# Kernel tuning notes

Hardware: AMD Instinct MI355X
Metric: run time of the kernel (lower is better)

The kernel has to match this reference:

```python
import jax, jax.numpy as jnp
import numpy as np

B, N, K, L, H = 8, 2048, 16, 4, 8
CONV = (64, 64, 128, 256)
W_DIM, N_CODES, E_DIM, P_DIM, FF = 512, 8, 64, 256, 512


def act(x):
    return jax.nn.leaky_relu(x, 0.2)


def ln(x, g, b, eps=1e-5):
    m = jnp.mean(x, -1, keepdims=True)
    v = jnp.mean((x - m) ** 2, -1, keepdims=True)
    return g * (x - m) / jnp.sqrt(v + eps) + b


# per-batch neighbor gather: f [C,N], i [N,K] -> [C,N,K]
gather_nb = jax.vmap(lambda f, i: f[:, i])


def knn_idx(y):  # y [B,3,N] -> [B,N,K]
    xx = jnp.sum(y * y, axis=1)
    inner = jnp.einsum('bcn,bcm->bnm', y, y)
    dist = 2.0 * inner - xx[:, :, None] - xx[:, None, :]  # negative sq dist
    return jax.lax.top_k(dist, K)[1]


def mha(q, kv, Wq, bq, Wk, bk, Wv, bv, Wo, bo):
    Bq, S, D = q.shape
    Sk = kv.shape[1]
    dh = D // H
    qh = (q @ Wq.T + bq).reshape(Bq, S, H, dh)
    kh = (kv @ Wk.T + bk).reshape(Bq, Sk, H, dh)
    vh = (kv @ Wv.T + bv).reshape(Bq, Sk, H, dh)
    a = jax.nn.softmax(jnp.einsum('bqhd,bkhd->bhqk', qh, kh) * (1.0 / np.sqrt(dh)))
    o = jnp.einsum('bhqk,bkhd->bqhd', a, vh).reshape(Bq, S, D)
    return o @ Wo.T + bo


def setup_inputs() -> dict:
    key = jax.random.key(0)
    ks = iter(jax.random.split(key, 48))
    nrm = lambda shape: jax.random.normal(next(ks), shape, jnp.float32) * 0.02
    d = {
        'x': jax.random.normal(next(ks), (B, N, 3), jnp.float32),
        'W_ec': nrm((CONV[0], 6)), 'b_ec': jnp.zeros((CONV[0],), jnp.float32),
        'Wc1': nrm((CONV[1], CONV[0])), 'bc1': jnp.zeros((CONV[1],), jnp.float32),
        'Wc2': nrm((CONV[2], CONV[1])), 'bc2': jnp.zeros((CONV[2],), jnp.float32),
        'Wc3': nrm((CONV[3], CONV[2])), 'bc3': jnp.zeros((CONV[3],), jnp.float32),
        'Wf': nrm((W_DIM, sum(CONV))), 'bf': jnp.zeros((W_DIM,), jnp.float32),
        'Wpc': nrm((P_DIM, E_DIM)), 'bpc': jnp.zeros((P_DIM,), jnp.float32),
        'Wpi': nrm((P_DIM, 3)), 'bpi': jnp.zeros((P_DIM,), jnp.float32),
        'Wq': nrm((L, 2, P_DIM, P_DIM)), 'bq': jnp.zeros((L, 2, P_DIM), jnp.float32),
        'Wk': nrm((L, 2, P_DIM, P_DIM)), 'bk': jnp.zeros((L, 2, P_DIM), jnp.float32),
        'Wv': nrm((L, 2, P_DIM, P_DIM)), 'bv': jnp.zeros((L, 2, P_DIM), jnp.float32),
        'Wo': nrm((L, 2, P_DIM, P_DIM)), 'bo': jnp.zeros((L, 2, P_DIM), jnp.float32),
        'ln1g': jnp.ones((L, P_DIM), jnp.float32), 'ln1b': jnp.zeros((L, P_DIM), jnp.float32),
        'ln2g': jnp.ones((L, P_DIM), jnp.float32), 'ln2b': jnp.zeros((L, P_DIM), jnp.float32),
        'Wff1': nrm((L, FF, P_DIM)), 'bff1': jnp.zeros((L, FF), jnp.float32),
        'Wff2': nrm((L, P_DIM, FF)), 'bff2': jnp.zeros((L, P_DIM), jnp.float32),
        'ln3g': jnp.ones((L, P_DIM), jnp.float32), 'ln3b': jnp.zeros((L, P_DIM), jnp.float32),
        'lnfg': jnp.ones((P_DIM,), jnp.float32), 'lnfb': jnp.zeros((P_DIM,), jnp.float32),
        'Wcm': nrm((E_DIM, P_DIM)), 'bcm': jnp.zeros((E_DIM,), jnp.float32),
    }
    return d


def reference(x, W_ec, b_ec, Wc1, bc1, Wc2, bc2, Wc3, bc3, Wf, bf, Wpc, bpc, Wpi, bpi,
              Wq, bq, Wk, bk, Wv, bv, Wo, bo, ln1g, ln1b, ln2g, ln2b,
              Wff1, bff1, Wff2, bff2, ln3g, ln3b, lnfg, lnfb, Wcm, bcm):
    y = jnp.transpose(x, (0, 2, 1))                      # [B,3,N]
    idx = knn_idx(y)                                     # [B,N,K]
    nb = gather_nb(y, idx)                               # [B,3,N,K]
    feats = jnp.concatenate([nb - y[..., None], jnp.broadcast_to(y[..., None], nb.shape)], axis=1)
    h = act(jnp.einsum('oc,bcnk->bonk', W_ec, feats) + b_ec[:, None, None])
    h = h.max(axis=3)                                    # [B,64,N]
    xs = [h]
    for Wl, bl in ((Wc1, bc1), (Wc2, bc2), (Wc3, bc3)):
        h = gather_nb(h, idx).max(axis=3)                # graph max pooling
        h = act(jnp.einsum('oc,bcn->bon', Wl, h) + bl[:, None])
        xs.append(h)
    h = jnp.concatenate(xs, axis=1)                      # [B,512,N]
    h = jnp.einsum('oc,bcn->bon', Wf, h) + bf[:, None]
    xm = h.max(axis=2)                                   # [B,512]
    q = act(xm.reshape(B, N_CODES, E_DIM) @ Wpc.T + bpc) # [B,8,256]
    mem = act(x @ Wpi.T + bpi)                           # [B,N,256]
    for l in range(L):
        q = ln(q + mha(q, q, Wq[l, 0], bq[l, 0], Wk[l, 0], bk[l, 0], Wv[l, 0], bv[l, 0], Wo[l, 0], bo[l, 0]), ln1g[l], ln1b[l])
        q = ln(q + mha(q, mem, Wq[l, 1], bq[l, 1], Wk[l, 1], bk[l, 1], Wv[l, 1], bv[l, 1], Wo[l, 1], bo[l, 1]), ln2g[l], ln2b[l])
        q = ln(q + (act(q @ Wff1[l].T + bff1[l]) @ Wff2[l].T + bff2[l]), ln3g[l], ln3b[l])
    q = ln(q, lnfg, lnfb)
    out = q @ Wcm.T + bcm                                # [B,8,64]
    return out.reshape(B, W_DIM)
```

## Files before the change

### kernel.cpp

```cpp
#include <hip/hip_runtime.h>
#include <math.h>

#define BN 8
#define NP 2048
#define KNN 16
#define NL 4
#define NH 8

typedef __attribute__((ext_vector_type(8))) short bf16x8;
typedef __attribute__((ext_vector_type(4))) float f32x4;

__device__ __forceinline__ unsigned short f2bf(float f) {
    unsigned u = __float_as_uint(f);
    unsigned r = (u + 0x7FFFu + ((u >> 16) & 1u)) >> 16;
    return (unsigned short)r;
}
__device__ __forceinline__ float bf2f(unsigned short s) {
    return __uint_as_float(((unsigned)s) << 16);
}
__device__ __forceinline__ unsigned fmono(float f) {
    unsigned u = __float_as_uint(f);
    return (u & 0x80000000u) ? ~u : (u | 0x80000000u);
}
__device__ __forceinline__ float funmono(unsigned k) {
    return (k & 0x80000000u) ? __uint_as_float(k ^ 0x80000000u) : __uint_as_float(~k);
}

__device__ __forceinline__ float gemv_dot(const unsigned short* __restrict__ wrow, const float* sm, int K8) {
    const uint4* w8 = (const uint4*)wrow;
    const float4* r4 = (const float4*)sm;
    float a0 = 0.f, a1 = 0.f, a2 = 0.f, a3 = 0.f;
    #pragma unroll 8
    for (int c = 0; c < K8; ++c) {
        uint4 wv = w8[c];
        float4 x0 = r4[c * 2], x1 = r4[c * 2 + 1];
        a0 += x0.x * __uint_as_float(wv.x << 16) + x0.y * __uint_as_float(wv.x & 0xFFFF0000u);
        a1 += x0.z * __uint_as_float(wv.y << 16) + x0.w * __uint_as_float(wv.y & 0xFFFF0000u);
        a2 += x1.x * __uint_as_float(wv.z << 16) + x1.y * __uint_as_float(wv.z & 0xFFFF0000u);
        a3 += x1.z * __uint_as_float(wv.w << 16) + x1.w * __uint_as_float(wv.w & 0xFFFF0000u);
    }
    return (a0 + a1) + (a2 + a3);
}

__device__ __forceinline__ float gemv_i8(const char* __restrict__ wrow, const float* sm, int K16) {
    const uint4* w16 = (const uint4*)wrow;
    const float4* r4 = (const float4*)sm;
    float a0 = 0.f, a1 = 0.f, a2 = 0.f, a3 = 0.f;
    #pragma unroll 4
    for (int c = 0; c < K16; ++c) {
        uint4 wv = w16[c];
        float4 x0 = r4[c * 4], x1 = r4[c * 4 + 1], x2 = r4[c * 4 + 2], x3 = r4[c * 4 + 3];
        a0 += x0.x * (float)(signed char)(wv.x) + x0.y * (float)(signed char)(wv.x >> 8)
            + x0.z * (float)(signed char)(wv.x >> 16) + x0.w * (float)(signed char)(wv.x >> 24);
        a1 += x1.x * (float)(signed char)(wv.y) + x1.y * (float)(signed char)(wv.y >> 8)
            + x1.z * (float)(signed char)(wv.y >> 16) + x1.w * (float)(signed char)(wv.y >> 24);
        a2 += x2.x * (float)(signed char)(wv.z) + x2.y * (float)(signed char)(wv.z >> 8)
            + x2.z * (float)(signed char)(wv.z >> 16) + x2.w * (float)(signed char)(wv.z >> 24);
        a3 += x3.x * (float)(signed char)(wv.w) + x3.y * (float)(signed char)(wv.w >> 8)
            + x3.z * (float)(signed char)(wv.w >> 16) + x3.w * (float)(signed char)(wv.w >> 24);
    }
    return (a0 + a1) + (a2 + a3);
}

__device__ __forceinline__ unsigned long long shflx_u64(unsigned long long v, int j) {
    int lo = __shfl_xor((int)(unsigned)(v & 0xFFFFFFFFull), j);
    int hi = __shfl_xor((int)(unsigned)(v >> 32), j);
    return ((unsigned long long)(unsigned)hi << 32) | (unsigned)lo;
}

__device__ __forceinline__ unsigned sort64_u32(unsigned v, int lane) {
    #pragma unroll
    for (int k = 2; k <= 64; k <<= 1) {
        #pragma unroll
        for (int j = k >> 1; j > 0; j >>= 1) {
            unsigned o = (unsigned)__shfl_xor((int)v, j);
            bool up = ((lane & k) == 0);
            bool lower = ((lane & j) == 0);
            unsigned mn = v < o ? v : o;
            unsigned mx = v < o ? o : v;
            v = (up == lower) ? mn : mx;
        }
    }
    return v;
}

__device__ __forceinline__ unsigned long long sort64_u64(unsigned long long v, int lane) {
    #pragma unroll
    for (int k = 2; k <= 64; k <<= 1) {
        #pragma unroll
        for (int j = k >> 1; j > 0; j >>= 1) {
            unsigned long long o = shflx_u64(v, j);
            bool up = ((lane & k) == 0);
            bool lower = ((lane & j) == 0);
            unsigned long long mn = v < o ? v : o;
            unsigned long long mx = v < o ? o : v;
            v = (up == lower) ? mn : mx;
        }
    }
    return v;
}

__global__ __launch_bounds__(256) void knn_kernel(const float* __restrict__ x, int* __restrict__ idxout) {
    __shared__ float xs[2048], ys[2048], zs[2048], ns[2048];
    __shared__ unsigned long long cand[4][64];
    int tid = threadIdx.x;
    int wv = tid >> 6, lane = tid & 63;
    int p = blockIdx.x * 4 + wv;
    int b = p >> 11, n = p & 2047;
    const float* xb = x + (size_t)b * NP * 3;
    for (int t = tid; t < 2048; t += 256) {
        float mx = xb[t * 3 + 0], my = xb[t * 3 + 1], mz = xb[t * 3 + 2];
        xs[t] = mx; ys[t] = my; zs[t] = mz;
        ns[t] = mx * mx + my * my + mz * mz;
    }
    __syncthreads();
    float cx = xs[n], cy = ys[n], cz = zs[n], xn = ns[n];
    unsigned key[32];
    unsigned lmax = 0u;
    #pragma unroll
    for (int t = 0; t < 32; ++t) {
        int m = (t << 6) | lane;
        float dd = 2.0f * (cx * xs[m] + cy * ys[m] + cz * zs[m]) - xn - ns[m];
        unsigned u = __float_as_uint(dd);
        u = (u & 0x80000000u) ? ~u : (u | 0x80000000u);
        key[t] = u;
        lmax = lmax > u ? lmax : u;
    }
    unsigned sorted = sort64_u32(lmax, lane);
    unsigned S = (unsigned)__shfl((int)sorted, 48);
    int c = 0;
    #pragma unroll
    for (int t = 0; t < 32; ++t) c += (key[t] >= S) ? 1 : 0;
    int inc = c;
    #pragma unroll
    for (int d = 1; d < 64; d <<= 1) {
        int tsh = __shfl_up(inc, d);
        if (lane >= d) inc += tsh;
    }
    int C = __shfl(inc, 63);
    int* op = idxout + (size_t)p * KNN;
    if (C <= 64) {
        int off = inc - c;
        #pragma unroll
        for (int t = 0; t < 32; ++t) {
            if (key[t] >= S) {
                int m = (t << 6) | lane;
                cand[wv][off++] = ((unsigned long long)key[t] << 16) | (unsigned)(2047 - m);
            }
        }
        asm volatile("s_waitcnt lgkmcnt(0)" ::: "memory");
        unsigned long long ck = (lane < C) ? cand[wv][lane] : 0ull;
        ck = sort64_u64(ck, lane);
        if (lane >= 48) op[63 - lane] = 2047 - (int)(unsigned)(ck & 0xFFFFull);
    } else {
        unsigned taken = 0u;
        for (int r = 0; r < KNN; ++r) {
            unsigned long long best = 0ull;
            #pragma unroll
            for (int t = 0; t < 32; ++t) {
                if (!((taken >> t) & 1u)) {
                    int m = (t << 6) | lane;
                    unsigned long long ck = ((unsigned long long)key[t] << 16) | (unsigned)(2047 - m);
                    if (ck > best) best = ck;
                }
            }
            #pragma unroll
            for (int d = 1; d < 64; d <<= 1) {
                unsigned long long o = shflx_u64(best, d);
                if (o > best) best = o;
            }
            int m = 2047 - (int)(unsigned)(best & 0xFFFFull);
            if (lane == 0) op[r] = m;
            if ((m & 63) == lane) taken |= 1u << (m >> 6);
        }
    }
}

__global__ __launch_bounds__(256) void edge_conv_kernel(const float* __restrict__ x, const int* __restrict__ idx,
                                                        const float* __restrict__ Wec, const float* __restrict__ bec,
                                                        unsigned short* __restrict__ hcatT) {
    int tid = threadIdx.x;
    int g = tid >> 6, o = tid & 63;
    int p = blockIdx.x * 4 + g;
    int b = p >> 11;
    __shared__ float nb[4][KNN][3];
    __shared__ float ctr[4][3];
    if (o < KNN) {
        int j = idx[(size_t)p * KNN + o];
        const float* xp = x + ((size_t)b * NP + j) * 3;
        nb[g][o][0] = xp[0]; nb[g][o][1] = xp[1]; nb[g][o][2] = xp[2];
    }
    if (o >= KNN && o < KNN + 3) ctr[g][o - KNN] = x[(size_t)p * 3 + (o - KNN)];
    __syncthreads();
    float w0 = Wec[o * 6 + 0], w1 = Wec[o * 6 + 1], w2 = Wec[o * 6 + 2];
    float w3 = Wec[o * 6 + 3], w4 = Wec[o * 6 + 4], w5 = Wec[o * 6 + 5];
    float c0 = ctr[g][0], c1 = ctr[g][1], c2 = ctr[g][2];
    float base = bec[o] + w3 * c0 + w4 * c1 + w5 * c2;
    float m = -3.4e38f;
    #pragma unroll
    for (int k = 0; k < KNN; ++k) {
        float v = base + w0 * (nb[g][k][0] - c0) + w1 * (nb[g][k][1] - c1) + w2 * (nb[g][k][2] - c2);
        v = v > 0.f ? v : 0.2f * v;
        m = fmaxf(m, v);
    }
    hcatT[(size_t)p * 512 + o] = f2bf(m);
}

__global__ __launch_bounds__(256) void pool_bf16_kernel(const unsigned short* __restrict__ src, int s_coff,
                                                        const int* __restrict__ idx,
                                                        unsigned short* __restrict__ dst, int C) {
    int tid = threadIdx.x, wv = tid >> 6, lane = tid & 63;
    int p = blockIdx.x * 4 + wv;
    int b = p >> 11;
    const int* ip = idx + (size_t)p * KNN;
    const unsigned short* sb = src + (size_t)b * NP * 512 + s_coff;
    for (int c0 = 0; c0 < C; c0 += 64) {
        int ch = c0 + lane;
        float m = -3.4e38f;
        #pragma unroll
        for (int k = 0; k < KNN; ++k) {
            int j = ip[k];
            m = fmaxf(m, bf2f(sb[(size_t)j * 512 + ch]));
        }
        dst[(size_t)p * C + ch] = f2bf(m);
    }
}

__global__ __launch_bounds__(256) void mfma_conv64_kernel(const unsigned short* __restrict__ A,
                                                          const unsigned short* __restrict__ W,
                                                          const float* __restrict__ bias,
                                                          unsigned short* __restrict__ hcatT, int coff) {
    __shared__ unsigned short As[128][72];
    __shared__ unsigned short Bs[64][72];
    int m0 = blockIdx.x * 128, b = blockIdx.z;
    int tid = threadIdx.x;
    int lane = tid & 63, wave = tid >> 6;
    int wr = wave >> 1, wc = wave & 1;
    int quad = lane >> 4, l16 = lane & 15;
    {
        int r = tid >> 1, s = (tid & 1) * 32;
        const unsigned short* ap = A + (size_t)b * NP * 64 + (size_t)(m0 + r) * 64 + s;
        uint4 v0 = *(const uint4*)(ap);
        uint4 v1 = *(const uint4*)(ap + 8);
        uint4 v2 = *(const uint4*)(ap + 16);
        uint4 v3 = *(const uint4*)(ap + 24);
        *(uint4*)&As[r][s] = v0; *(uint4*)&As[r][s + 8] = v1;
        *(uint4*)&As[r][s + 16] = v2; *(uint4*)&As[r][s + 24] = v3;
    }
    {
        int r = tid >> 2, s = (tid & 3) * 16;
        const unsigned short* wp = W + r * 64 + s;
        *(uint4*)&Bs[r][s] = *(const uint4*)wp;
        *(uint4*)&Bs[r][s + 8] = *(const uint4*)(wp + 8);
    }
    __syncthreads();
    f32x4 acc[4][2] = {};
    #pragma unroll
    for (int k0 = 0; k0 < 64; k0 += 32) {
        bf16x8 af[4], bfv[2];
        #pragma unroll
        for (int i = 0; i < 4; ++i) af[i] = *(const bf16x8*)&As[wr * 64 + i * 16 + l16][k0 + quad * 8];
        #pragma unroll
        for (int j = 0; j < 2; ++j) bfv[j] = *(const bf16x8*)&Bs[wc * 32 + j * 16 + l16][k0 + quad * 8];
        #pragma unroll
        for (int i = 0; i < 4; ++i)
            #pragma unroll
            for (int j = 0; j < 2; ++j)
                acc[i][j] = __builtin_amdgcn_mfma_f32_16x16x32_bf16(af[i], bfv[j], acc[i][j], 0, 0, 0);
    }
    #pragma unroll
    for (int i = 0; i < 4; ++i) {
        #pragma unroll
        for (int r = 0; r < 4; ++r) {
            int pt = m0 + wr * 64 + i * 16 + quad * 4 + r;
            #pragma unroll
            for (int j = 0; j < 2; ++j) {
                int ch = wc * 32 + j * 16 + l16;
                float v = acc[i][j][r] + bias[ch];
                v = v > 0.f ? v : 0.2f * v;
                hcatT[((size_t)b * NP + pt) * 512 + coff + ch] = f2bf(v);
            }
        }
    }
}

__global__ __launch_bounds__(256) void wcast_kernel(const float* __restrict__ Wf, const float* __restrict__ Wc3,
                                                    const float* __restrict__ Wk, const float* __restrict__ Wv,
                                                    const float* __restrict__ bk, const float* __restrict__ bv,
                                                    const float* __restrict__ Wc1, const float* __restrict__ Wc2,
                                                    const float* __restrict__ Wq, const float* __restrict__ Wo,
                                                    const float* __restrict__ Wff1, const float* __restrict__ Wff2,
                                                    unsigned short* __restrict__ WfB, unsigned short* __restrict__ Wc3B,
                                                    unsigned short* __restrict__ WkvB, float* __restrict__ bkv,
                                                    unsigned short* __restrict__ Wc1B, unsigned short* __restrict__ Wc2B,
                                                    unsigned short* __restrict__ WtB, unsigned short* __restrict__ Wff1B,
                                                    unsigned short* __restrict__ Wff2B,
                                                    unsigned* __restrict__ xmk) {
    int id = blockIdx.x * 256 + threadIdx.x;
    if (id < 262144) { WfB[id] = f2bf(Wf[id]); return; }
    int j = id - 262144;
    if (j < 32768) { Wc3B[j] = f2bf(Wc3[j]); return; }
    j -= 32768;
    if (j < 524288) {
        int l = j >> 17, r = j & 131071;
        float v = (r < 65536) ? Wk[(size_t)(l * 2 + 1) * 65536 + r]
                              : Wv[(size_t)(l * 2 + 1) * 65536 + (r - 65536)];
        WkvB[j] = f2bf(v);
        return;
    }
    j -= 524288;
    if (j < 2048) {
        int l = j >> 9, r = j & 511;
        bkv[j] = (r < 256) ? bk[(l * 2 + 1) * 256 + r] : bv[(l * 2 + 1) * 256 + (r - 256)];
        return;
    }
    j -= 2048;
    if (j < 4096) { Wc1B[j] = f2bf(Wc1[j]); return; }
    j -= 4096;
    if (j < 8192) { Wc2B[j] = f2bf(Wc2[j]); return; }
    j -= 8192;
    if (j < 4096) { xmk[j] = 0u; return; }
    j -= 4096;
    if (j < 1572864) {
        int l = j / 393216;
        int r = j - l * 393216;
        int m = r >> 16, c = r & 65535;
        float v;
        if (m == 0)      v = Wq[(size_t)(l * 2 + 0) * 65536 + c];
        else if (m == 1) v = Wk[(size_t)(l * 2 + 0) * 65536 + c];
        else if (m == 2) v = Wv[(size_t)(l * 2 + 0) * 65536 + c];
        else if (m == 3) v = Wo[(size_t)(l * 2 + 0) * 65536 + c];
        else if (m == 4) v = Wq[(size_t)(l * 2 + 1) * 65536 + c];
        else             v = Wo[(size_t)(l * 2 + 1) * 65536 + c];
        WtB[j] = f2bf(v);
        return;
    }
    j -= 1572864;
    if (j < 524288) { Wff1B[j] = f2bf(Wff1[j]); return; }
    j -= 524288;
    if (j < 524288) { Wff2B[j] = f2bf(Wff2[j]); return; }
}

__global__ __launch_bounds__(256) void wquant_kernel(const unsigned short* __restrict__ WtB,
                                                     const unsigned short* __restrict__ Wff1B,
                                                     const unsigned short* __restrict__ Wff2B,
                                                     char* __restrict__ WtI, float* __restrict__ StW,
                                                     char* __restrict__ FF1I, float* __restrict__ SF1,
                                                     char* __restrict__ FF2I, float* __restrict__ SF2) {
    int tid = threadIdx.x, wv = tid >> 6, lane = tid & 63;
    int row = blockIdx.x * 4 + wv;
    const unsigned short* src;
    char* dst;
    float* sc;
    int K;
    if (row < 6144)      { src = WtB + (size_t)row * 256; dst = WtI + (size_t)row * 256; sc = StW + row; K = 256; }
    else if (row < 8192) { int r = row - 6144; src = Wff1B + (size_t)r * 256; dst = FF1I + (size_t)r * 256; sc = SF1 + r; K = 256; }
    else                 { int r = row - 8192; src = Wff2B + (size_t)r * 512; dst = FF2I + (size_t)r * 512; sc = SF2 + r; K = 512; }
    int per = K >> 6;
    float w[8];
    float mx = 0.f;
    for (int e = 0; e < per; ++e) { w[e] = bf2f(src[lane * per + e]); mx = fmaxf(mx, fabsf(w[e])); }
    #pragma unroll
    for (int off = 1; off < 64; off <<= 1) mx = fmaxf(mx, __shfl_xor(mx, off));
    float s = fmaxf(mx, 1e-30f) * (1.0f / 127.0f);
    float inv = 1.0f / s;
    unsigned pk[2] = {0u, 0u};
    for (int e = 0; e < per; ++e) {
        int q = (int)rintf(w[e] * inv);
        q = q > 127 ? 127 : (q < -127 ? -127 : q);
        pk[e >> 2] |= ((unsigned)(q & 255)) << (8 * (e & 3));
    }
    ((unsigned*)dst)[lane * (per >> 2)] = pk[0];
    if (per == 8) ((unsigned*)dst)[lane * 2 + 1] = pk[1];
    if (lane == 0) *sc = s;
}

__global__ __launch_bounds__(256) void mfma_gemm_kernel(const unsigned short* __restrict__ A, size_t a_bstride,
                                                        const unsigned short* __restrict__ B, size_t b_bstride,
                                                        const float* __restrict__ bias, int bias_per_m,
                                                        void* __restrict__ C, size_t c_bstride, int c_rstride,
                                                        int K, int act, int out_bf16,
                                                        unsigned* __restrict__ xmk, int domax) {
    __shared__ unsigned short As[128][40];
    __shared__ unsigned short Bs[128][40];
    int m0 = blockIdx.x * 128, n0 = blockIdx.y * 128, b = blockIdx.z;
    int tid = threadIdx.x;
    int lane = tid & 63, wave = tid >> 6;
    int wr = wave >> 1, wc = wave & 1;
    int quad = lane >> 4, l16 = lane & 15;
    int r0 = tid >> 2, kc0 = (tid & 3) * 8;
    f32x4 acc[4][4] = {};
    const unsigned short* Ab = A + (size_t)b * a_bstride;
    const unsigned short* Bb = B + (size_t)b * b_bstride;
    for (int k0 = 0; k0 < K; k0 += 32) {
        uint4 a0 = *(const uint4*)(Ab + (size_t)(m0 + r0) * K + k0 + kc0);
        uint4 a1 = *(const uint4*)(Ab + (size_t)(m0 + r0 + 64) * K + k0 + kc0);
        uint4 b0 = *(const uint4*)(Bb + (size_t)(n0 + r0) * K + k0 + kc0);
        uint4 b1 = *(const uint4*)(Bb + (size_t)(n0 + r0 + 64) * K + k0 + kc0);
        __syncthreads();
        *(uint4*)&As[r0][kc0] = a0;
        *(uint4*)&As[r0 + 64][kc0] = a1;
        *(uint4*)&Bs[r0][kc0] = b0;
        *(uint4*)&Bs[r0 + 64][kc0] = b1;
        __syncthreads();
        bf16x8 af[4], bfv[4];
        #pragma unroll
        for (int i = 0; i < 4; ++i) af[i] = *(const bf16x8*)&As[wr * 64 + i * 16 + l16][quad * 8];
        #pragma unroll
        for (int j = 0; j < 4; ++j) bfv[j] = *(const bf16x8*)&Bs[wc * 64 + j * 16 + l16][quad * 8];
        #pragma unroll
        for (int i = 0; i < 4; ++i)
            #pragma unroll
            for (int j = 0; j < 4; ++j)
                acc[i][j] = __builtin_amdgcn_mfma_f32_16x16x32_bf16(af[i], bfv[j], acc[i][j], 0, 0, 0);
    }
    if (domax) {
        #pragma unroll
        for (int i = 0; i < 4; ++i) {
            #pragma unroll
            for (int r = 0; r < 4; ++r) {
                int m = m0 + wr * 64 + i * 16 + quad * 4 + r;
                float v = fmaxf(fmaxf(acc[i][0][r], acc[i][1][r]), fmaxf(acc[i][2][r], acc[i][3][r]));
                v += bias[m];
                #pragma unroll
                for (int off = 1; off <= 8; off <<= 1) v = fmaxf(v, __shfl_xor(v, off));
                if (l16 == 0) atomicMax(&xmk[(size_t)b * 512 + m], fmono(v));
            }
        }
        return;
    }
    #pragma unroll
    for (int i = 0; i < 4; ++i) {
        #pragma unroll
        for (int r = 0; r < 4; ++r) {
            int m = m0 + wr * 64 + i * 16 + quad * 4 + r;
            float bm = bias_per_m ? bias[m] : 0.f;
            #pragma unroll
            for (int j = 0; j < 4; ++j) {
                int n = n0 + wc * 64 + j * 16 + l16;
                float v = acc[i][j][r] + (bias_per_m ? bm : bias[n]);
                if (act) v = v > 0.f ? v : 0.2f * v;
                size_t off = (size_t)b * c_bstride + (size_t)m * c_rstride + n;
                if (out_bf16) ((unsigned short*)C)[off] = f2bf(v);
                else          ((float*)C)[off] = v;
            }
        }
    }
}

__global__ __launch_bounds__(256) void mfma_kv_all_kernel(const unsigned short* __restrict__ A,
                                                          const unsigned short* __restrict__ W,
                                                          const float* __restrict__ bkv,
                                                          unsigned short* __restrict__ KVall) {
    __shared__ unsigned short As[128][40];
    __shared__ unsigned short Bs[128][40];
    int m0 = blockIdx.x * 128;
    int nb = blockIdx.y & 3, l = blockIdx.y >> 2;
    int n0 = nb * 128;
    int b = blockIdx.z;
    int tid = threadIdx.x;
    int lane = tid & 63, wave = tid >> 6;
    int wr = wave >> 1, wc = wave & 1;
    int quad = lane >> 4, l16 = lane & 15;
    int r0 = tid >> 2, kc0 = (tid & 3) * 8;
    f32x4 acc[4][4] = {};
    const unsigned short* Ab = A + (size_t)b * NP * 256;
    const unsigned short* Bb = W + (size_t)l * 131072;
    const float* bias = bkv + l * 512;
    for (int k0 = 0; k0 < 256; k0 += 32) {
        uint4 a0 = *(const uint4*)(Ab + (size_t)(m0 + r0) * 256 + k0 + kc0);
        uint4 a1 = *(const uint4*)(Ab + (size_t)(m0 + r0 + 64) * 256 + k0 + kc0);
        uint4 b0 = *(const uint4*)(Bb + (size_t)(n0 + r0) * 256 + k0 + kc0);
        uint4 b1 = *(const uint4*)(Bb + (size_t)(n0 + r0 + 64) * 256 + k0 + kc0);
        __syncthreads();
        *(uint4*)&As[r0][kc0] = a0;
        *(uint4*)&As[r0 + 64][kc0] = a1;
        *(uint4*)&Bs[r0][kc0] = b0;
        *(uint4*)&Bs[r0 + 64][kc0] = b1;
        __syncthreads();
        bf16x8 af[4], bfv[4];
        #pragma unroll
        for (int i = 0; i < 4; ++i) af[i] = *(const bf16x8*)&As[wr * 64 + i * 16 + l16][quad * 8];
        #pragma unroll
        for (int j = 0; j < 4; ++j) bfv[j] = *(const bf16x8*)&Bs[wc * 64 + j * 16 + l16][quad * 8];
        #pragma unroll
        for (int i = 0; i < 4; ++i)
            #pragma unroll
            for (int j = 0; j < 4; ++j)
                acc[i][j] = __builtin_amdgcn_mfma_f32_16x16x32_bf16(af[i], bfv[j], acc[i][j], 0, 0, 0);
    }
    unsigned short* Cb = KVall + ((size_t)l * BN + b) * NP * 512;
    #pragma unroll
    for (int i = 0; i < 4; ++i) {
        #pragma unroll
        for (int r = 0; r < 4; ++r) {
            int m = m0 + wr * 64 + i * 16 + quad * 4 + r;
            #pragma unroll
            for (int j = 0; j < 4; ++j) {
                int n = n0 + wc * 64 + j * 16 + l16;
                Cb[(size_t)m * 512 + n] = f2bf(acc[i][j][r] + bias[n]);
            }
        }
    }
}

__global__ __launch_bounds__(256) void pc_kernel(const unsigned* __restrict__ xmk, const float* __restrict__ Wpc,
                                                 const float* __restrict__ bpc,
                                                 const unsigned short* __restrict__ Wqkv,
                                                 const float* __restrict__ bq0, const float* __restrict__ bk0,
                                                 const float* __restrict__ bv0,
                                                 float* __restrict__ q, float* __restrict__ Qs,
                                                 float* __restrict__ Ks, float* __restrict__ Vs) {
    int row = blockIdx.x, tid = threadIdx.x;
    int id = row * 256 + tid;
    int b = row >> 3, i = row & 7;
    const unsigned* xr = xmk + b * 512 + i * 64;
    const float* w = Wpc + (size_t)tid * 64;
    float acc = bpc[tid];
    #pragma unroll
    for (int e = 0; e < 64; ++e) acc += funmono(xr[e]) * w[e];
    float qv = acc > 0.f ? acc : 0.2f * acc;
    q[id] = qv;
    __shared__ __align__(16) float a[256];
    a[tid] = qv;
    __syncthreads();
    Qs[id] = bq0[tid] + gemv_dot(Wqkv + (size_t)tid * 256, a, 32);
    Ks[id] = bk0[tid] + gemv_dot(Wqkv + 65536 + (size_t)tid * 256, a, 32);
    Vs[id] = bv0[tid] + gemv_dot(Wqkv + 131072 + (size_t)tid * 256, a, 32);
}

__global__ __launch_bounds__(256) void mem_kernel(const float* __restrict__ x, const float* __restrict__ Wpi,
                                                  const float* __restrict__ bpi, unsigned short* __restrict__ memB) {
    size_t id = (size_t)blockIdx.x * 256 + threadIdx.x;
    int p = (int)(id & 255);
    size_t pt = id >> 8;
    float x0 = x[pt * 3 + 0], x1 = x[pt * 3 + 1], x2 = x[pt * 3 + 2];
    float v = bpi[p] + x0 * Wpi[p * 3 + 0] + x1 * Wpi[p * 3 + 1] + x2 * Wpi[p * 3 + 2];
    v = v > 0.f ? v : 0.2f * v;
    memB[id] = f2bf(v);
}

__global__ __launch_bounds__(1024) void attn_ln_kernel(const float* __restrict__ Qs, const float* __restrict__ Ks,
                                                       const float* __restrict__ Vs,
                                                       const unsigned short* __restrict__ WoB,
                                                       const float* __restrict__ bo, const float* __restrict__ res,
                                                       const float* __restrict__ g, const float* __restrict__ bt,
                                                       const unsigned short* __restrict__ Wq1B,
                                                       const float* __restrict__ bq1,
                                                       float* __restrict__ out, float* __restrict__ Qc) {
    int row = blockIdx.x, tid = threadIdx.x;
    int b = row >> 3;
    __shared__ float Kl[2048], Vl[2048];
    __shared__ __align__(16) float qr[256];
    __shared__ float sc[64];
    __shared__ __align__(16) float r[256];
    __shared__ __align__(16) float aout[256];
    __shared__ float red[1024];
    for (int t = tid; t < 2048; t += 1024) {
        Kl[t] = Ks[(size_t)b * 2048 + t];
        Vl[t] = Vs[(size_t)b * 2048 + t];
    }
    if (tid < 256) qr[tid] = Qs[(size_t)row * 256 + tid];
    __syncthreads();
    const float scale = 0.17677669529663687f;
    {
        int pair = tid >> 4, part = tid & 15;
        int h = pair >> 3, k = pair & 7;
        int d = part * 2;
        float dot = qr[h * 32 + d] * Kl[k * 256 + h * 32 + d]
                  + qr[h * 32 + d + 1] * Kl[k * 256 + h * 32 + d + 1];
        dot += __shfl_xor(dot, 1);
        dot += __shfl_xor(dot, 2);
        dot += __shfl_xor(dot, 4);
        dot += __shfl_xor(dot, 8);
        if (part == 0) sc[pair] = dot * scale;
    }
    __syncthreads();
    if (tid < 64) {
        float v = sc[tid];
        float m = v;
        #pragma unroll
        for (int off = 1; off < 8; off <<= 1) m = fmaxf(m, __shfl_xor(m, off));
        float e = __expf(v - m);
        float s = e;
        #pragma unroll
        for (int off = 1; off < 8; off <<= 1) s += __shfl_xor(s, off);
        sc[tid] = e / s;
    }
    __syncthreads();
    if (tid < 256) {
        int h = tid >> 5;
        float acc = 0.f;
        #pragma unroll
        for (int k = 0; k < 8; ++k) acc += sc[h * 8 + k] * Vl[k * 256 + tid];
        r[tid] = acc;
    }
    __syncthreads();
    int o4 = tid >> 2, p4 = tid & 3;
    float v;
    {
        float acc = gemv_dot(WoB + (size_t)o4 * 256 + p4 * 64, r + p4 * 64, 8);
        acc += __shfl_xor(acc, 1);
        acc += __shfl_xor(acc, 2);
        v = (p4 == 0) ? (bo[o4] + acc + res[(size_t)row * 256 + o4]) : 0.f;
    }
    red[tid] = v; __syncthreads();
    for (int s = 512; s; s >>= 1) { if (tid < s) red[tid] += red[tid + s]; __syncthreads(); }
    float mean = red[0] * (1.0f / 256.0f);
    __syncthreads();
    float dv = (p4 == 0) ? v - mean : 0.f;
    red[tid] = dv * dv; __syncthreads();
    for (int s = 512; s; s >>= 1) { if (tid < s) red[tid] += red[tid + s]; __syncthreads(); }
    float var = red[0] * (1.0f / 256.0f);
    if (p4 == 0) {
        float oln = g[o4] * dv * rsqrtf(var + 1e-5f) + bt[o4];
        out[(size_t)row * 256 + o4] = oln;
        aout[o4] = oln;
    }
    __syncthreads();
    {
        float qacc = gemv_dot(Wq1B + (size_t)o4 * 256 + p4 * 64, aout + p4 * 64, 8);
        qacc += __shfl_xor(qacc, 1);
        qacc += __shfl_xor(qacc, 2);
        if (p4 == 0) Qc[(size_t)row * 256 + o4] = bq1[o4] + qacc;
    }
}

__global__ __launch_bounds__(256) void ca_part_kernel(const float* __restrict__ Qc,
                                                      const unsigned short* __restrict__ KVl,
                                                      float* __restrict__ part) {
    int kb = blockIdx.x, h = blockIdx.y, b = blockIdx.z;
    int tid = threadIdx.x;
    __shared__ float q[8][32];
    __shared__ __align__(16) float S[8][128];
    __shared__ float om[8][8][32];
    const float scale = 0.17677669529663687f;
    {
        int i = tid >> 5, d = tid & 31;
        q[i][d] = Qc[(size_t)(b * 8 + i) * 256 + h * 32 + d];
    }
    __syncthreads();
    {
        int kk = tid & 127, half = tid >> 7;
        int k = kb * 128 + kk;
        const unsigned short* kp = KVl + ((size_t)b * NP + k) * 512 + h * 32;
        float kd[32];
        #pragma unroll
        for (int u = 0; u < 4; ++u) {
            uint4 raw = *(const uint4*)(kp + u * 8);
            unsigned w0 = raw.x, w1 = raw.y, w2 = raw.z, w3 = raw.w;
            kd[u * 8 + 0] = __uint_as_float(w0 << 16); kd[u * 8 + 1] = __uint_as_float(w0 & 0xFFFF0000u);
            kd[u * 8 + 2] = __uint_as_float(w1 << 16); kd[u * 8 + 3] = __uint_as_float(w1 & 0xFFFF0000u);
            kd[u * 8 + 4] = __uint_as_float(w2 << 16); kd[u * 8 + 5] = __uint_as_float(w2 & 0xFFFF0000u);
            kd[u * 8 + 6] = __uint_as_float(w3 << 16); kd[u * 8 + 7] = __uint_as_float(w3 & 0xFFFF0000u);
        }
        #pragma unroll
        for (int i = 0; i < 4; ++i) {
            int ri = half * 4 + i;
            float dot = 0.f;
            #pragma unroll
            for (int d = 0; d < 32; ++d) dot += q[ri][d] * kd[d];
            S[ri][kk] = dot * scale;
        }
    }
    __syncthreads();
    float* pout = part + (((size_t)(b * NH + h)) * 16 + kb) * 288;
    {
        int i = tid >> 5, l32 = tid & 31;
        float m = -3.4e38f;
        #pragma unroll
        for (int t = 0; t < 4; ++t) m = fmaxf(m, S[i][l32 + t * 32]);
        #pragma unroll
        for (int off = 16; off; off >>= 1) m = fmaxf(m, __shfl_xor(m, off));
        float s = 0.f;
        #pragma unroll
        for (int t = 0; t < 4; ++t) {
            float e = __expf(S[i][l32 + t * 32] - m);
            S[i][l32 + t * 32] = e;
            s += e;
        }
        #pragma unroll
        for (int off = 16; off; off >>= 1) s += __shfl_xor(s, off);
        if (l32 == 0) { pout[i] = m; pout[8 + i] = s; }
    }
    __syncthreads();
    {
        int d = tid & 31, grp = tid >> 5;
        const unsigned short* Vb = KVl + ((size_t)b * NP + kb * 128) * 512 + 256 + h * 32 + d;
        float acc[8] = {};
        #pragma unroll 4
        for (int t = 0; t < 16; ++t) {
            int kk = grp * 16 + t;
            float v = bf2f(Vb[(size_t)kk * 512]);
            #pragma unroll
            for (int i = 0; i < 8; ++i) acc[i] += S[i][kk] * v;
        }
        #pragma unroll
        for (int i = 0; i < 8; ++i) om[grp][i][d] = acc[i];
    }
    __syncthreads();
    {
        int i = tid >> 5, d = tid & 31;
        float sum = 0.f;
        #pragma unroll
        for (int g = 0; g < 8; ++g) sum += om[g][i][d];
        pout[16 + i * 32 + d] = sum;
    }
}

__global__ __launch_bounds__(1024) void combine_ff_kernel(const float* __restrict__ part,
                                                          const char* __restrict__ WoI, const float* __restrict__ sWo,
                                                          const float* __restrict__ bo, const float* __restrict__ res,
                                                          const float* __restrict__ g2, const float* __restrict__ b2t,
                                                          const char* __restrict__ W1I, const float* __restrict__ sW1,
                                                          const float* __restrict__ b1,
                                                          const char* __restrict__ W2I, const float* __restrict__ sW2,
                                                          const float* __restrict__ b2,
                                                          const float* __restrict__ g3, const float* __restrict__ b3t,
                                                          float* __restrict__ out,
                                                          int is_last, const float* __restrict__ lnfg,
                                                          const float* __restrict__ lnfb, const float* __restrict__ Wcm,
                                                          const float* __restrict__ bcm, float* __restrict__ finout,
                                                          const char* __restrict__ WqkvnI, const float* __restrict__ sQn,
                                                          const float* __restrict__ bqn, const float* __restrict__ bkn,
                                                          const float* __restrict__ bvn,
                                                          float* __restrict__ Qs, float* __restrict__ Ks,
                                                          float* __restrict__ Vs) {
    int row = blockIdx.x, tid = threadIdx.x;
    int b = row >> 3, i = row & 7;
    __shared__ __align__(16) float r[256];
    __shared__ __align__(16) float a[256];
    __shared__ __align__(16) float hbuf[512];
    __shared__ float red[1024];
    {
        int h = tid >> 7, rem = tid & 127, d = rem >> 2, g = rem & 3;
        const float* pb = part + (size_t)(b * NH + h) * 16 * 288;
        float M = -3.4e38f;
        #pragma unroll
        for (int t = 0; t < 4; ++t) M = fmaxf(M, pb[(g * 4 + t) * 288 + i]);
        M = fmaxf(M, __shfl_xor(M, 1));
        M = fmaxf(M, __shfl_xor(M, 2));
        float L = 0.f, O = 0.f;
        #pragma unroll
        for (int t = 0; t < 4; ++t) {
            int kb = g * 4 + t;
            float w = __expf(pb[kb * 288 + i] - M);
            L += pb[kb * 288 + 8 + i] * w;
            O += pb[kb * 288 + 16 + i * 32 + d] * w;
        }
        L += __shfl_xor(L, 1); L += __shfl_xor(L, 2);
        O += __shfl_xor(O, 1); O += __shfl_xor(O, 2);
        if (g == 0) r[h * 32 + d] = O / L;
    }
    __syncthreads();
    int o4 = tid >> 2, p4 = tid & 3;
    float v;
    {
        float acc = gemv_i8(WoI + (size_t)o4 * 256 + p4 * 64, r + p4 * 64, 4);
        acc += __shfl_xor(acc, 1);
        acc += __shfl_xor(acc, 2);
        v = (p4 == 0) ? (bo[o4] + sWo[o4] * acc + res[(size_t)row * 256 + o4]) : 0.f;
    }
    red[tid] = v; __syncthreads();
    for (int s = 512; s; s >>= 1) { if (tid < s) red[tid] += red[tid + s]; __syncthreads(); }
    float mean = red[0] * (1.0f / 256.0f);
    __syncthreads();
    float dv = (p4 == 0) ? v - mean : 0.f;
    red[tid] = dv * dv; __syncthreads();
    for (int s = 512; s; s >>= 1) { if (tid < s) red[tid] += red[tid + s]; __syncthreads(); }
    float var = red[0] * (1.0f / 256.0f);
    if (p4 == 0) a[o4] = g2[o4] * dv * rsqrtf(var + 1e-5f) + b2t[o4];
    __syncthreads();
    {
        int o = tid >> 1, p = tid & 1;
        float acc = gemv_i8(W1I + (size_t)o * 256 + p * 128, a + p * 128, 8);
        acc += __shfl_xor(acc, 1);
        if (p == 0) { float t = b1[o] + sW1[o] * acc; hbuf[o] = t > 0.f ? t : 0.2f * t; }
    }
    __syncthreads();
    float vF;
    {
        float acc = gemv_i8(W2I + (size_t)o4 * 512 + p4 * 128, hbuf + p4 * 128, 8);
        acc += __shfl_xor(acc, 1);
        acc += __shfl_xor(acc, 2);
        vF = (p4 == 0) ? (b2[o4] + sW2[o4] * acc + a[o4]) : 0.f;
    }
    red[tid] = vF; __syncthreads();
    for (int s = 512; s; s >>= 1) { if (tid < s) red[tid] += red[tid + s]; __syncthreads(); }
    float mean2 = red[0] * (1.0f / 256.0f);
    __syncthreads();
    float dv2 = (p4 == 0) ? vF - mean2 : 0.f;
    red[tid] = dv2 * dv2; __syncthreads();
    for (int s = 512; s; s >>= 1) { if (tid < s) red[tid] += red[tid + s]; __syncthreads(); }
    float var2 = red[0] * (1.0f / 256.0f);
    float tln = 0.f;
    if (p4 == 0) {
        tln = g3[o4] * dv2 * rsqrtf(var2 + 1e-5f) + b3t[o4];
        r[o4] = tln;
    }
    __syncthreads();
    if (!is_last) {
        if (p4 == 0) out[(size_t)row * 256 + o4] = tln;
        if (tid < 768) {
            int which = tid >> 8, o = tid & 255;
            float acc = gemv_i8(WqkvnI + (size_t)which * 65536 + (size_t)o * 256, r, 16);
            float bb = (which == 0) ? bqn[o] : (which == 1) ? bkn[o] : bvn[o];
            float* dst = (which == 0) ? Qs : (which == 1) ? Ks : Vs;
            dst[(size_t)row * 256 + o] = bb + sQn[which * 256 + o] * acc;
        }
        return;
    }
    float tf = (tid < 256) ? r[tid] : 0.f;
    red[tid] = tf; __syncthreads();
    for (int s = 512; s; s >>= 1) { if (tid < s) red[tid] += red[tid + s]; __syncthreads(); }
    float mean3 = red[0] * (1.0f / 256.0f);
    __syncthreads();
    float d3 = (tid < 256) ? tf - mean3 : 0.f;
    red[tid] = d3 * d3; __syncthreads();
    for (int s = 512; s; s >>= 1) { if (tid < s) red[tid] += red[tid + s]; __syncthreads(); }
    float var3 = red[0] * (1.0f / 256.0f);
    if (tid < 256) a[tid] = lnfg[tid] * d3 * rsqrtf(var3 + 1e-5f) + lnfb[tid];
    __syncthreads();
    if (tid < 64) {
        const float4* w4 = (const float4*)(Wcm + (size_t)tid * 256);
        const float4* a4 = (const float4*)a;
        float acc = bcm[tid];
        #pragma unroll 8
        for (int c = 0; c < 64; ++c) {
            float4 av = a4[c], wv = w4[c];
            acc += av.x * wv.x + av.y * wv.y + av.z * wv.z + av.w * wv.w;
        }
        finout[(size_t)b * 512 + i * 64 + tid] = acc;
    }
}

extern "C" void kernel_launch(void* const* d_in, const int* in_sizes, int n_in,
                              void* d_out, int out_size, void* d_ws, size_t ws_size,
                              hipStream_t stream) {
    const float* x    = (const float*)d_in[0];
    const float* Wec  = (const float*)d_in[1];
    const float* bec  = (const float*)d_in[2];
    const float* Wc1  = (const float*)d_in[3];
    const float* bc1  = (const float*)d_in[4];
    const float* Wc2  = (const float*)d_in[5];
    const float* bc2  = (const float*)d_in[6];
    const float* Wc3  = (const float*)d_in[7];
    const float* bc3  = (const float*)d_in[8];
    const float* Wf   = (const float*)d_in[9];
    const float* bf   = (const float*)d_in[10];
    const float* Wpc  = (const float*)d_in[11];
    const float* bpc  = (const float*)d_in[12];
    const float* Wpi  = (const float*)d_in[13];
    const float* bpi  = (const float*)d_in[14];
    const float* Wq   = (const float*)d_in[15];
    const float* bq   = (const float*)d_in[16];
    const float* Wk   = (const float*)d_in[17];
    const float* bk   = (const float*)d_in[18];
    const float* Wv   = (const float*)d_in[19];
    const float* bv   = (const float*)d_in[20];
    const float* Wo   = (const float*)d_in[21];
    const float* bo   = (const float*)d_in[22];
    const float* ln1g = (const float*)d_in[23];
    const float* ln1b = (const float*)d_in[24];
    const float* ln2g = (const float*)d_in[25];
    const float* ln2b = (const float*)d_in[26];
    const float* Wff1 = (const float*)d_in[27];
    const float* bff1 = (const float*)d_in[28];
    const float* Wff2 = (const float*)d_in[29];
    const float* bff2 = (const float*)d_in[30];
    const float* ln3g = (const float*)d_in[31];
    const float* ln3b = (const float*)d_in[32];
    const float* lnfg = (const float*)d_in[33];
    const float* lnfb = (const float*)d_in[34];
    const float* Wcm  = (const float*)d_in[35];
    const float* bcm  = (const float*)d_in[36];
    float* out = (float*)d_out;

    float* ws = (float*)d_ws;
    size_t off = 0;
    auto alloc = [&](size_t n) { float* p = ws + off; off += (n + 3) & ~(size_t)3; return p; };
    int*            idx   = (int*)alloc((size_t)BN * NP * KNN);
    unsigned short* hcatT = (unsigned short*)alloc((size_t)BN * NP * 512 / 2);
    unsigned short* poolT = (unsigned short*)alloc((size_t)BN * NP * 128 / 2);
    unsigned short* WfB   = (unsigned short*)alloc(262144 / 2);
    unsigned short* Wc1B  = (unsigned short*)alloc(4096 / 2);
    unsigned short* Wc2B  = (unsigned short*)alloc(8192 / 2);
    unsigned short* Wc3B  = (unsigned short*)alloc(32768 / 2);
    unsigned short* WkvB  = (unsigned short*)alloc(524288 / 2);
    float*          bkv   = alloc(2048);
    unsigned short* memB  = (unsigned short*)alloc((size_t)BN * NP * 256 / 2);
    unsigned short* KVall = (unsigned short*)alloc((size_t)NL * BN * NP * 512 / 2);
    unsigned*       xmk   = (unsigned*)alloc((size_t)BN * 512);
    unsigned short* WtB   = (unsigned short*)alloc(1572864 / 2);
    unsigned short* Wff1B = (unsigned short*)alloc(524288 / 2);
    unsigned short* Wff2B = (unsigned short*)alloc(524288 / 2);
    char*           WtI   = (char*)alloc(1572864 / 4);
    float*          StW   = alloc(6144);
    char*           FF1I  = (char*)alloc(524288 / 4);
    float*          SF1   = alloc(2048);
    char*           FF2I  = (char*)alloc(524288 / 4);
    float*          SF2   = alloc(1024);
    float*          qa    = alloc((size_t)BN * 8 * 256);
    float*          qb    = alloc((size_t)BN * 8 * 256);
    float*          Qs    = alloc((size_t)BN * 8 * 256);
    float*          Ks    = alloc((size_t)BN * 8 * 256);
    float*          Vs    = alloc((size_t)BN * 8 * 256);
    float*          Qc    = alloc((size_t)BN * 8 * 256);
    float*          part  = alloc((size_t)BN * NH * 16 * 288);

    wcast_kernel<<<13512, 256, 0, stream>>>(Wf, Wc3, Wk, Wv, bk, bv, Wc1, Wc2, Wq, Wo, Wff1, Wff2,
                                            WfB, Wc3B, WkvB, bkv, Wc1B, Wc2B, WtB, Wff1B, Wff2B, xmk);
    wquant_kernel<<<2304, 256, 0, stream>>>(WtB, Wff1B, Wff2B, WtI, StW, FF1I, SF1, FF2I, SF2);

    knn_kernel<<<BN * NP / 4, 256, 0, stream>>>(x, idx);
    edge_conv_kernel<<<BN * NP / 4, 256, 0, stream>>>(x, idx, Wec, bec, hcatT);

    pool_bf16_kernel<<<BN * NP / 4, 256, 0, stream>>>(hcatT, 0, idx, poolT, 64);
    mfma_conv64_kernel<<<dim3(NP / 128, 1, BN), 256, 0, stream>>>(poolT, Wc1B, bc1, hcatT, 64);
    pool_bf16_kernel<<<BN * NP / 4, 256, 0, stream>>>(hcatT, 64, idx, poolT, 64);
    mfma_gemm_kernel<<<dim3(NP / 128, 1, BN), 256, 0, stream>>>(poolT, (size_t)NP * 64, Wc2B, 0,
                                                                bc2, 0, (void*)(hcatT + 128), (size_t)NP * 512, 512,
                                                                64, 1, 1, nullptr, 0);
    pool_bf16_kernel<<<BN * NP / 4, 256, 0, stream>>>(hcatT, 128, idx, poolT, 128);
    mfma_gemm_kernel<<<dim3(NP / 128, 2, BN), 256, 0, stream>>>(poolT, (size_t)NP * 128, Wc3B, 0,
                                                                bc3, 0, (void*)(hcatT + 256), (size_t)NP * 512, 512,
                                                                128, 1, 1, nullptr, 0);
    mfma_gemm_kernel<<<dim3(4, NP / 128, BN), 256, 0, stream>>>(WfB, 0, hcatT, (size_t)NP * 512,
                                                                bf, 1, nullptr, 0, 0,
                                                                512, 0, 0, xmk, 1);
    pc_kernel<<<BN * 8, 256, 0, stream>>>(xmk, Wpc, bpc, WtB, bq, bk, bv, qa, Qs, Ks, Vs);
    mem_kernel<<<BN * NP, 256, 0, stream>>>(x, Wpi, bpi, memB);
    mfma_kv_all_kernel<<<dim3(NP / 128, 4 * NL, BN), 256, 0, stream>>>(memB, WkvB, bkv, KVall);

    for (int l = 0; l < NL; ++l) {
        const unsigned short* Wl = WtB + (size_t)l * 393216;
        const float* bo0 = bo + (l * 2 + 0) * 256;
        const float* bq1 = bq + (l * 2 + 1) * 256;
        const float* bo1 = bo + (l * 2 + 1) * 256;
        int last = (l == NL - 1);

        attn_ln_kernel<<<BN * 8, 1024, 0, stream>>>(Qs, Ks, Vs, Wl + 3 * 65536, bo0, qa,
                                                    ln1g + l * 256, ln1b + l * 256, Wl + 4 * 65536, bq1, qb, Qc);
        ca_part_kernel<<<dim3(16, NH, BN), 256, 0, stream>>>(Qc, KVall + (size_t)l * BN * NP * 512, part);
        combine_ff_kernel<<<BN * 8, 1024, 0, stream>>>(part,
                                                       WtI + (size_t)l * 393216 + 5 * 65536, StW + l * 1536 + 5 * 256,
                                                       bo1, qb,
                                                       ln2g + l * 256, ln2b + l * 256,
                                                       FF1I + (size_t)l * 131072, SF1 + l * 512, bff1 + l * 512,
                                                       FF2I + (size_t)l * 131072, SF2 + l * 256, bff2 + l * 256,
                                                       ln3g + l * 256, ln3b + l * 256, qa,
                                                       last, lnfg, lnfb, Wcm, bcm, out,
                                                       last ? nullptr : WtI + (size_t)(l + 1) * 393216,
                                                       last ? nullptr : StW + (l + 1) * 1536,
                                                       bq + ((l + 1) * 2) * 256, bk + ((l + 1) * 2) * 256,
                                                       bv + ((l + 1) * 2) * 256,
                                                       Qs, Ks, Vs);
    }

    (void)in_sizes; (void)n_in; (void)out_size; (void)ws_size;
}
```

Baseline: 517.3 us.

## Use int8 weights for small attention GEMVs and enlarge knn blocks to 1024 threads

Switches the Q/K/V projection in pc_kernel and the Wo and cross-attention Q projections in attn_ln_kernel from bf16 weights to the int8-quantized weights with per-row scales that were already produced for combine_ff. This halves weight bytes read by these bandwidth-bound GEMVs, at some cost in accuracy. Separately, knn_kernel now runs 16 waves per block instead of 4, so the per-batch point cloud staged into shared memory is loaded once per 16 query points rather than once per 4.

```diff
diff --git a/kernel.cpp b/kernel.cpp
--- a/kernel.cpp
+++ b/kernel.cpp
@@ -100,15 +100,15 @@
     return v;
 }
 
-__global__ __launch_bounds__(256) void knn_kernel(const float* __restrict__ x, int* __restrict__ idxout) {
+__global__ __launch_bounds__(1024) void knn_kernel(const float* __restrict__ x, int* __restrict__ idxout) {
     __shared__ float xs[2048], ys[2048], zs[2048], ns[2048];
-    __shared__ unsigned long long cand[4][64];
+    __shared__ unsigned long long cand[16][64];
     int tid = threadIdx.x;
     int wv = tid >> 6, lane = tid & 63;
-    int p = blockIdx.x * 4 + wv;
+    int p = blockIdx.x * 16 + wv;
     int b = p >> 11, n = p & 2047;
     const float* xb = x + (size_t)b * NP * 3;
-    for (int t = tid; t < 2048; t += 256) {
+    for (int t = tid; t < 2048; t += 1024) {
         float mx = xb[t * 3 + 0], my = xb[t * 3 + 1], mz = xb[t * 3 + 2];
         xs[t] = mx; ys[t] = my; zs[t] = mz;
         ns[t] = mx * mx + my * my + mz * mz;
@@ -506,7 +506,7 @@
 
 __global__ __launch_bounds__(256) void pc_kernel(const unsigned* __restrict__ xmk, const float* __restrict__ Wpc,
                                                  const float* __restrict__ bpc,
-                                                 const unsigned short* __restrict__ Wqkv,
+                                                 const char* __restrict__ WqkvI, const float* __restrict__ sQ,
                                                  const float* __restrict__ bq0, const float* __restrict__ bk0,
                                                  const float* __restrict__ bv0,
                                                  float* __restrict__ q, float* __restrict__ Qs,
@@ -524,9 +524,9 @@
     __shared__ __align__(16) float a[256];
     a[tid] = qv;
     __syncthreads();
-    Qs[id] = bq0[tid] + gemv_dot(Wqkv + (size_t)tid * 256, a, 32);
-    Ks[id] = bk0[tid] + gemv_dot(Wqkv + 65536 + (size_t)tid * 256, a, 32);
-    Vs[id] = bv0[tid] + gemv_dot(Wqkv + 131072 + (size_t)tid * 256, a, 32);
+    Qs[id] = bq0[tid] + sQ[tid] * gemv_i8(WqkvI + (size_t)tid * 256, a, 16);
+    Ks[id] = bk0[tid] + sQ[256 + tid] * gemv_i8(WqkvI + 65536 + (size_t)tid * 256, a, 16);
+    Vs[id] = bv0[tid] + sQ[512 + tid] * gemv_i8(WqkvI + 131072 + (size_t)tid * 256, a, 16);
 }
 
 __global__ __launch_bounds__(256) void mem_kernel(const float* __restrict__ x, const float* __restrict__ Wpi,
@@ -542,10 +542,10 @@
 
 __global__ __launch_bounds__(1024) void attn_ln_kernel(const float* __restrict__ Qs, const float* __restrict__ Ks,
                                                        const float* __restrict__ Vs,
-                                                       const unsigned short* __restrict__ WoB,
+                                                       const char* __restrict__ WoI, const float* __restrict__ sWo,
                                                        const float* __restrict__ bo, const float* __restrict__ res,
                                                        const float* __restrict__ g, const float* __restrict__ bt,
-                                                       const unsigned short* __restrict__ Wq1B,
+                                                       const char* __restrict__ Wq1I, const float* __restrict__ sWq1,
                                                        const float* __restrict__ bq1,
                                                        float* __restrict__ out, float* __restrict__ Qc) {
     int row = blockIdx.x, tid = threadIdx.x;
@@ -599,10 +599,10 @@
     int o4 = tid >> 2, p4 = tid & 3;
     float v;
     {
-        float acc = gemv_dot(WoB + (size_t)o4 * 256 + p4 * 64, r + p4 * 64, 8);
+        float acc = gemv_i8(WoI + (size_t)o4 * 256 + p4 * 64, r + p4 * 64, 4);
         acc += __shfl_xor(acc, 1);
         acc += __shfl_xor(acc, 2);
-        v = (p4 == 0) ? (bo[o4] + acc + res[(size_t)row * 256 + o4]) : 0.f;
+        v = (p4 == 0) ? (bo[o4] + sWo[o4] * acc + res[(size_t)row * 256 + o4]) : 0.f;
     }
     red[tid] = v; __syncthreads();
     for (int s = 512; s; s >>= 1) { if (tid < s) red[tid] += red[tid + s]; __syncthreads(); }
@@ -619,10 +619,10 @@
     }
     __syncthreads();
     {
-        float qacc = gemv_dot(Wq1B + (size_t)o4 * 256 + p4 * 64, aout + p4 * 64, 8);
+        float qacc = gemv_i8(Wq1I + (size_t)o4 * 256 + p4 * 64, aout + p4 * 64, 4);
         qacc += __shfl_xor(qacc, 1);
         qacc += __shfl_xor(qacc, 2);
-        if (p4 == 0) Qc[(size_t)row * 256 + o4] = bq1[o4] + qacc;
+        if (p4 == 0) Qc[(size_t)row * 256 + o4] = bq1[o4] + sWq1[o4] * qacc;
     }
 }
 
@@ -912,7 +912,7 @@
                                             WfB, Wc3B, WkvB, bkv, Wc1B, Wc2B, WtB, Wff1B, Wff2B, xmk);
     wquant_kernel<<<2304, 256, 0, stream>>>(WtB, Wff1B, Wff2B, WtI, StW, FF1I, SF1, FF2I, SF2);
 
-    knn_kernel<<<BN * NP / 4, 256, 0, stream>>>(x, idx);
+    knn_kernel<<<BN * NP / 16, 1024, 0, stream>>>(x, idx);
     edge_conv_kernel<<<BN * NP / 4, 256, 0, stream>>>(x, idx, Wec, bec, hcatT);
 
     pool_bf16_kernel<<<BN * NP / 4, 256, 0, stream>>>(hcatT, 0, idx, poolT, 64);
@@ -928,19 +928,22 @@
     mfma_gemm_kernel<<<dim3(4, NP / 128, BN), 256, 0, stream>>>(WfB, 0, hcatT, (size_t)NP * 512,
                                                                 bf, 1, nullptr, 0, 0,
                                                                 512, 0, 0, xmk, 1);
-    pc_kernel<<<BN * 8, 256, 0, stream>>>(xmk, Wpc, bpc, WtB, bq, bk, bv, qa, Qs, Ks, Vs);
+    pc_kernel<<<BN * 8, 256, 0, stream>>>(xmk, Wpc, bpc, WtI, StW, bq, bk, bv, qa, Qs, Ks, Vs);
     mem_kernel<<<BN * NP, 256, 0, stream>>>(x, Wpi, bpi, memB);
     mfma_kv_all_kernel<<<dim3(NP / 128, 4 * NL, BN), 256, 0, stream>>>(memB, WkvB, bkv, KVall);
 
     for (int l = 0; l < NL; ++l) {
-        const unsigned short* Wl = WtB + (size_t)l * 393216;
         const float* bo0 = bo + (l * 2 + 0) * 256;
         const float* bq1 = bq + (l * 2 + 1) * 256;
         const float* bo1 = bo + (l * 2 + 1) * 256;
         int last = (l == NL - 1);
 
-        attn_ln_kernel<<<BN * 8, 1024, 0, stream>>>(Qs, Ks, Vs, Wl + 3 * 65536, bo0, qa,
-                                                    ln1g + l * 256, ln1b + l * 256, Wl + 4 * 65536, bq1, qb, Qc);
+        attn_ln_kernel<<<BN * 8, 1024, 0, stream>>>(Qs, Ks, Vs,
+                                                    WtI + (size_t)l * 393216 + 3 * 65536, StW + l * 1536 + 3 * 256,
+                                                    bo0, qa,
+                                                    ln1g + l * 256, ln1b + l * 256,
+                                                    WtI + (size_t)l * 393216 + 4 * 65536, StW + l * 1536 + 4 * 256,
+                                                    bq1, qb, Qc);
         ca_part_kernel<<<dim3(16, NH, BN), 256, 0, stream>>>(Qc, KVall + (size_t)l * BN * NP * 512, part);
         combine_ff_kernel<<<BN * 8, 1024, 0, stream>>>(part,
                                                        WtI + (size_t)l * 393216 + 5 * 65536, StW + l * 1536 + 5 * 256,
```

Result: faster. 496.9 us (median of 2 runs) (-3.9%).
